# Performance work log

Measured on AMD Instinct MI355X. Metric: run time of the kernel, lower is better.

The kernel has to match this reference:

```python
import jax, jax.numpy as jnp
import numpy as np

B, N, S = 4, 16384, 16384
C1, C2 = 256, 256
D_MODEL, NHEAD, OUT_DIM = 256, 8, 256
HEAD_DIM = D_MODEL // NHEAD
EPS_ATTN = 1e-6


def _layernorm(x, g, b, eps=1e-5):
    mu = jnp.mean(x, axis=-1, keepdims=True)
    var = jnp.mean(jnp.square(x - mu), axis=-1, keepdims=True)
    return (x - mu) * jax.lax.rsqrt(var + eps) * g + b


def setup_inputs() -> dict:
    key = jax.random.key(0)
    ks = jax.random.split(key, 20)
    def w(k, shape, fan_in):
        return jax.random.normal(k, shape, jnp.float32) * (1.0 / np.sqrt(fan_in))
    return {
        "feat1": jax.random.normal(ks[0], (B, C1, N), jnp.float32),
        "xyz1": jax.random.normal(ks[1], (B, N, 3), jnp.float32),
        "feat2": jax.random.normal(ks[2], (B, C2, S), jnp.float32),
        "xyz2": jax.random.normal(ks[3], (B, S, 3), jnp.float32),
        # pos_mlp2: Linear(3, d_model) -> ReLU -> Linear(d_model, feat2_dim)
        "pos_w1": w(ks[4], (D_MODEL, 3), 3),
        "pos_b1": jnp.zeros((D_MODEL,), jnp.float32),
        "pos_w2": w(ks[5], (C2, D_MODEL), D_MODEL),
        "pos_b2": jnp.zeros((C2,), jnp.float32),
        "q_w": w(ks[6], (D_MODEL, C1), C1),
        "k_w": w(ks[7], (D_MODEL, C2), C2),
        "v_w": w(ks[8], (D_MODEL, C2), C2),
        "merge_w": w(ks[9], (D_MODEL, D_MODEL), D_MODEL),
        # mlp: Linear(C1 + d_model, 2*d_model) -> ReLU -> Linear(2*d_model, out_dim)
        "mlp_w1": w(ks[10], (2 * D_MODEL, C1 + D_MODEL), C1 + D_MODEL),
        "mlp_w2": w(ks[11], (OUT_DIM, 2 * D_MODEL), 2 * D_MODEL),
        "ln1_g": jnp.ones((D_MODEL,), jnp.float32),
        "ln1_b": jnp.zeros((D_MODEL,), jnp.float32),
        "ln2_g": jnp.ones((OUT_DIM,), jnp.float32),
        "ln2_b": jnp.zeros((OUT_DIM,), jnp.float32),
    }


def reference(feat1, xyz1, feat2, xyz2, pos_w1, pos_b1, pos_w2, pos_b2,
              q_w, k_w, v_w, merge_w, mlp_w1, mlp_w2,
              ln1_g, ln1_b, ln2_g, ln2_b):
    bs = feat1.shape[0]
    f1 = jnp.transpose(feat1, (0, 2, 1))  # [B, N, C1]
    f2 = jnp.transpose(feat2, (0, 2, 1))  # [B, S, C2]
    # positional MLP on xyz2 added to feat2
    pos = jax.nn.relu(xyz2 @ pos_w1.T + pos_b1) @ pos_w2.T + pos_b2
    f2p = f2 + pos
    q = (f1 @ q_w.T).reshape(bs, -1, NHEAD, HEAD_DIM)   # [B, N, H, D]
    k = (f2 @ k_w.T).reshape(bs, -1, NHEAD, HEAD_DIM)   # [B, S, H, D]
    v = (f2p @ v_w.T).reshape(bs, -1, NHEAD, HEAD_DIM)  # [B, S, H, D]
    # Linear attention (elu feature map)
    Q = jax.nn.elu(q) + 1.0
    K = jax.nn.elu(k) + 1.0
    v_len = v.shape[1]
    V = v / v_len
    KV = jnp.einsum('nshd,nshv->nhdv', K, V)                 # [B, H, D, D]
    Z = 1.0 / (jnp.einsum('nlhd,nhd->nlh', Q, K.sum(axis=1)) + EPS_ATTN)
    msg = jnp.einsum('nlhd,nhdv,nlh->nlhv', Q, KV, Z) * v_len  # [B, N, H, D]
    msg = msg.reshape(bs, -1, NHEAD * HEAD_DIM) @ merge_w.T
    msg = _layernorm(msg, ln1_g, ln1_b)
    msg = jnp.concatenate([f1, msg], axis=2)
    msg = jax.nn.relu(msg @ mlp_w1.T) @ mlp_w2.T
    msg = _layernorm(msg, ln2_g, ln2_b)
    return jnp.transpose(msg, (0, 2, 1))  # [B, out_dim, N]
```

## Files before the change

kernel.cpp:

```cpp
#include <hip/hip_runtime.h>


typedef float f32x4 __attribute__((ext_vector_type(4)));
typedef __bf16 bf16x8 __attribute__((ext_vector_type(8)));
typedef __bf16 bf16x4 __attribute__((ext_vector_type(4)));

#define MFMA16(a, b, c) __builtin_amdgcn_mfma_f32_16x16x32_bf16((a), (b), (c), 0, 0, 0)

__device__ __forceinline__ void gll16(const __bf16* g, __bf16* l) {
    __builtin_amdgcn_global_load_lds(
        (const __attribute__((address_space(1))) void*)g,
        (__attribute__((address_space(3))) void*)l, 16, 0, 0);
}

__global__ __launch_bounds__(256) void prep_weights_kernel(
    const float* __restrict__ s0, const float* __restrict__ s1,
    const float* __restrict__ s2, const float* __restrict__ s3,
    const float* __restrict__ s4, const float* __restrict__ s5,
    const float* __restrict__ s6,
    __bf16* __restrict__ d0, __bf16* __restrict__ d1, __bf16* __restrict__ d2,
    __bf16* __restrict__ d3, __bf16* __restrict__ d4, __bf16* __restrict__ d5,
    __bf16* __restrict__ d6, float* __restrict__ zbase)
{
    int idx = blockIdx.x * 256 + threadIdx.x;
    if (idx < 327680) {
        int seg = idx >> 16, off = idx & 65535;
        const float* s = (seg == 0) ? s0 : (seg == 1) ? s1 : (seg == 2) ? s2 : (seg == 3) ? s3 : s4;
        __bf16* d = (seg == 0) ? d0 : (seg == 1) ? d1 : (seg == 2) ? d2 : (seg == 3) ? d3 : d4;
        d[off] = (__bf16)s[off];
    } else if (idx < 589824) {
        int off = idx - 327680; d5[off] = (__bf16)s5[off];
    } else if (idx < 720896) {
        int off = idx - 589824; d6[off] = (__bf16)s6[off];
    } else if (idx < 754688) {
        zbase[idx - 720896] = 0.f;
    }
}

__global__ __launch_bounds__(256) void pos_hidden_kernel(
    const float* __restrict__ xyz2, const float* __restrict__ pw1,
    const float* __restrict__ pb1, __bf16* __restrict__ Hid)
{
    const int tid = threadIdx.x;
    size_t tok = (size_t)blockIdx.x * 8 + (tid >> 5);
    int c0 = (tid & 31) * 8;
    const float* xz = xyz2 + tok * 3;
    float x = xz[0], y = xz[1], z = xz[2];
    bf16x8 o;
    #pragma unroll
    for (int j = 0; j < 8; ++j) {
        const float* wr = pw1 + (size_t)(c0 + j) * 3;
        float h = fmaf(x, wr[0], fmaf(y, wr[1], fmaf(z, wr[2], pb1[c0 + j])));
        o[j] = (__bf16)fmaxf(h, 0.f);
    }
    *(bf16x8*)(Hid + tok * 256 + c0) = o;
}

__global__ __launch_bounds__(256) void transpose_cast_kernel(
    const float* __restrict__ In, __bf16* __restrict__ Outb)
{
    const int tid = threadIdx.x;
    const int t0 = blockIdx.x * 64, c0 = blockIdx.y * 64;
    const size_t b = blockIdx.z;
    __shared__ __bf16 tile[64 * 72];
    #pragma unroll
    for (int i = 0; i < 4; ++i) {
        int c = i * 16 + (tid >> 4);
        int t4 = (tid & 15) * 4;
        float4 v = *(const float4*)(In + (b * 256 + c0 + c) * 16384 + t0 + t4);
        tile[(t4 + 0) * 72 + c] = (__bf16)v.x;
        tile[(t4 + 1) * 72 + c] = (__bf16)v.y;
        tile[(t4 + 2) * 72 + c] = (__bf16)v.z;
        tile[(t4 + 3) * 72 + c] = (__bf16)v.w;
    }
    __syncthreads();
    #pragma unroll
    for (int i = 0; i < 2; ++i) {
        int chunk = tid + i * 256;
        int tr = chunk >> 3, c8 = (chunk & 7) * 8;
        bf16x8 v = *(const bf16x8*)(tile + tr * 72 + c8);
        *(bf16x8*)(Outb + (b * 16384 + t0 + tr) * 256 + c0 + c8) = v;
    }
}

enum { EPI_STORE = 0, EPI_ELU = 1, EPI_ADDB = 2, EPI_RELU = 3, EPI_ELU_KSUM = 4 };

template <int EPI, bool SPLIT>
__global__ __launch_bounds__(256, 4) void gemm_tok(
    const __bf16* __restrict__ Wg,
    const __bf16* __restrict__ A0,
    const __bf16* __restrict__ A1,
    __bf16* __restrict__ Outg,
    const float* __restrict__ bias,
    const __bf16* __restrict__ addg,
    float* __restrict__ KSg,
    int K, int Cout)
{
    const int tid = threadIdx.x, w = tid >> 6, l = tid & 63, lm = l & 15;
    const int gm0 = blockIdx.x * 128, gn0 = blockIdx.y * 128;
    const size_t b = blockIdx.z;
    const __bf16* A0b = A0 + b * 16384 * (size_t)256;
    const __bf16* A1b = SPLIT ? (A1 + b * 16384 * (size_t)256) : nullptr;
    __bf16* Outb = Outg + b * 16384 * (size_t)Cout;
    const __bf16* addb = (EPI == EPI_ADDB) ? (addg + b * 16384 * (size_t)256) : nullptr;

    __shared__ __bf16 Alds[2][128 * 32];
    __shared__ __bf16 Wlds[2][128 * 32];
    __shared__ float kred[16 * 64];

    f32x4 acc[4][4];
    #pragma unroll
    for (int i = 0; i < 4; ++i)
        #pragma unroll
        for (int j = 0; j < 4; ++j) acc[i][j] = (f32x4){0.f, 0.f, 0.f, 0.f};

    const int wm = (w >> 1) * 64, wn = (w & 1) * 64;
    const int srow = tid >> 2, scol = (tid & 3) * 8;
    const int koff = (l >> 4) * 8;
    const int wbase = w * 512;

    auto stage = [&](int buf, int ks) {
        const __bf16* As = A0b; int kk = ks;
        if (SPLIT && ks >= 256) { As = A1b; kk = ks - 256; }
        gll16(As + (size_t)(gm0 + srow) * 256 + kk + scol,      &Alds[buf][wbase]);
        gll16(As + (size_t)(gm0 + 64 + srow) * 256 + kk + scol, &Alds[buf][2048 + wbase]);
        gll16(Wg + (size_t)(gn0 + srow) * K + ks + scol,        &Wlds[buf][wbase]);
        gll16(Wg + (size_t)(gn0 + 64 + srow) * K + ks + scol,   &Wlds[buf][2048 + wbase]);
    };

    stage(0, 0);
    __syncthreads();
    int cur = 0;
    for (int ks = 0; ks < K; ks += 32) {
        if (ks + 32 < K) stage(cur ^ 1, ks + 32);
        bf16x8 af[4], wf[4];
        #pragma unroll
        for (int mf = 0; mf < 4; ++mf)
            af[mf] = *(const bf16x8*)&Alds[cur][(wm + mf * 16 + lm) * 32 + koff];
        #pragma unroll
        for (int nf = 0; nf < 4; ++nf)
            wf[nf] = *(const bf16x8*)&Wlds[cur][(wn + nf * 16 + lm) * 32 + koff];
        #pragma unroll
        for (int mf = 0; mf < 4; ++mf)
            #pragma unroll
            for (int nf = 0; nf < 4; ++nf)
                acc[mf][nf] = MFMA16(af[mf], wf[nf], acc[mf][nf]);
        __syncthreads();
        cur ^= 1;
    }

    const int r0 = (l >> 4) * 4;
    float kpart[4] = {0.f, 0.f, 0.f, 0.f};
    #pragma unroll
    for (int mf = 0; mf < 4; ++mf) {
        #pragma unroll
        for (int nf = 0; nf < 4; ++nf) {
            int tok = gm0 + wm + mf * 16 + r0;
            int ch  = gn0 + wn + nf * 16 + lm;
            #pragma unroll
            for (int r = 0; r < 4; ++r) {
                float v = acc[mf][nf][r];
                if (EPI == EPI_ELU || EPI == EPI_ELU_KSUM)
                    v = (v > 0.f) ? (v + 1.f) : __expf(v);
                if (EPI == EPI_RELU) v = fmaxf(v, 0.f);
                if (EPI == EPI_ADDB) v = v + bias[ch] + (float)addb[(size_t)(tok + r) * 256 + ch];
                if (EPI == EPI_ELU_KSUM) kpart[nf] += v;
                Outb[(size_t)(tok + r) * Cout + ch] = (__bf16)v;
            }
        }
    }
    if (EPI == EPI_ELU_KSUM) {
        #pragma unroll
        for (int nf = 0; nf < 4; ++nf)
            kred[(w * 4 + (l >> 4)) * 64 + nf * 16 + lm] = kpart[nf];
        __syncthreads();
        if (tid < 128) {
            int c = tid;
            int wsel = (c >= 64) ? 1 : 0;
            float s = 0.f;
            #pragma unroll
            for (int q = 0; q < 4; ++q)
                s += kred[((wsel * 4) + q) * 64 + (c & 63)]
                   + kred[(((wsel + 2) * 4) + q) * 64 + (c & 63)];
            atomicAdd(&KSg[b * 256 + gn0 + c], s);
        }
    }
}

__global__ __launch_bounds__(256) void kv_kernel(
    const __bf16* __restrict__ Kb, const __bf16* __restrict__ Vb,
    float* __restrict__ KVg)
{
    const int tid = threadIdx.x, w = tid >> 6, l = tid & 63, lm = l & 15;
    const int sc = blockIdx.x, h = blockIdx.y, b = blockIdx.z;
    __shared__ __bf16 kT[32 * 264];
    __shared__ __bf16 vT[32 * 264];
    __shared__ float red[4 * 32 * 32];

    f32x4 acc[2][2];
    #pragma unroll
    for (int i = 0; i < 2; ++i)
        #pragma unroll
        for (int j = 0; j < 2; ++j) acc[i][j] = (f32x4){0.f, 0.f, 0.f, 0.f};

    const int koff = (l >> 4) * 8, r0 = (l >> 4) * 4;
    const size_t rowbase = (size_t)b * 16384;
    bf16x4 kreg[8], vreg[8];
    auto loadsub = [&](int sub) {
        int s0 = sc * 1024 + sub * 256;
        #pragma unroll
        for (int pass = 0; pass < 8; ++pass) {
            int sl = pass * 32 + (tid >> 3);
            int c4 = (tid & 7) * 4;
            kreg[pass] = *(const bf16x4*)(Kb + (rowbase + s0 + sl) * 256 + h * 32 + c4);
            vreg[pass] = *(const bf16x4*)(Vb + (rowbase + s0 + sl) * 256 + h * 32 + c4);
        }
    };
    loadsub(0);
    for (int sub = 0; sub < 4; ++sub) {
        __syncthreads();
        #pragma unroll
        for (int pass = 0; pass < 8; ++pass) {
            int sl = pass * 32 + (tid >> 3);
            int c4 = (tid & 7) * 4;
            #pragma unroll
            for (int i = 0; i < 4; ++i) {
                kT[(c4 + i) * 264 + sl] = kreg[pass][i];
                vT[(c4 + i) * 264 + sl] = vreg[pass][i];
            }
        }
        __syncthreads();
        if (sub < 3) loadsub(sub + 1);
        #pragma unroll
        for (int kq = 0; kq < 2; ++kq) {
            int sb = w * 64 + kq * 32;
            bf16x8 af[2], bfr[2];
            #pragma unroll
            for (int mf = 0; mf < 2; ++mf)
                af[mf] = *(const bf16x8*)(kT + (mf * 16 + lm) * 264 + sb + koff);
            #pragma unroll
            for (int nf = 0; nf < 2; ++nf)
                bfr[nf] = *(const bf16x8*)(vT + (nf * 16 + lm) * 264 + sb + koff);
            #pragma unroll
            for (int mf = 0; mf < 2; ++mf)
                #pragma unroll
                for (int nf = 0; nf < 2; ++nf)
                    acc[mf][nf] = MFMA16(af[mf], bfr[nf], acc[mf][nf]);
        }
    }
    #pragma unroll
    for (int mf = 0; mf < 2; ++mf)
        #pragma unroll
        for (int nf = 0; nf < 2; ++nf)
            #pragma unroll
            for (int r = 0; r < 4; ++r) {
                int d = mf * 16 + r0 + r, e = nf * 16 + lm;
                red[w * 1024 + d * 32 + e] = acc[mf][nf][r];
            }
    __syncthreads();
    #pragma unroll
    for (int i = 0; i < 4; ++i) {
        int idx = tid + i * 256;
        float s = red[idx] + red[1024 + idx] + red[2048 + idx] + red[3072 + idx];
        atomicAdd(&KVg[((size_t)(b * 8 + h)) * 1024 + idx], s);
    }
}

__global__ __launch_bounds__(256) void attn_apply(
    const __bf16* __restrict__ Qb, const float* __restrict__ KVg,
    const float* __restrict__ KSg, __bf16* __restrict__ Msg)
{
    const int tid = threadIdx.x, w = tid >> 6, l = tid & 63, lm = l & 15;
    const int tok0 = blockIdx.x * 64;
    const size_t b = blockIdx.y;
    __shared__ __bf16 kvT[8 * 32 * 40];
    __shared__ float ks_lds[256], z_lds[64 * 8];

    const float* KVb = KVg + b * 8192;
    #pragma unroll
    for (int i = 0; i < 32; ++i) {
        int idx = tid + i * 256;
        int h = idx >> 10, d = (idx >> 5) & 31, e = idx & 31;
        kvT[(h * 32 + e) * 40 + d] = (__bf16)KVb[idx];
    }
    ks_lds[tid] = KSg[b * 256 + tid];
    __syncthreads();

    const __bf16* Qbase = Qb + (b * 16384 + tok0) * (size_t)256;
    #pragma unroll
    for (int i = 0; i < 2; ++i) {
        int p = tid + i * 256;
        int tok = p >> 3, h = p & 7;
        const __bf16* qr = Qbase + (size_t)tok * 256 + h * 32;
        float s = 0.f;
        #pragma unroll
        for (int j = 0; j < 4; ++j) {
            bf16x8 q8 = *(const bf16x8*)(qr + j * 8);
            #pragma unroll
            for (int t = 0; t < 8; ++t) s += (float)q8[t] * ks_lds[h * 32 + j * 8 + t];
        }
        z_lds[tok * 8 + h] = 1.f / (s + 1e-6f);
    }
    __syncthreads();

    const int koff = (l >> 4) * 8, r0 = (l >> 4) * 4;
    const f32x4 zero4 = (f32x4){0.f, 0.f, 0.f, 0.f};
    #pragma unroll
    for (int h = 0; h < 8; ++h) {
        bf16x8 af = *(const bf16x8*)(Qbase + (size_t)(w * 16 + lm) * 256 + h * 32 + koff);
        #pragma unroll
        for (int nf = 0; nf < 2; ++nf) {
            bf16x8 bv = *(const bf16x8*)(kvT + (h * 32 + nf * 16 + lm) * 40 + koff);
            f32x4 m = MFMA16(af, bv, zero4);
            #pragma unroll
            for (int r = 0; r < 4; ++r) {
                int tok = w * 16 + r0 + r;
                Msg[(b * 16384 + tok0 + tok) * (size_t)256 + h * 32 + nf * 16 + lm] =
                    (__bf16)(m[r] * z_lds[tok * 8 + h]);
            }
        }
    }
}

template <bool TRANS>
__global__ __launch_bounds__(256, 2) void gemm_ln(
    const __bf16* __restrict__ Ag,
    const __bf16* __restrict__ Wg,
    const float* __restrict__ gv, const float* __restrict__ bv,
    __bf16* __restrict__ OutB,
    float* __restrict__ OutF,
    int K)
{
    const int tid = threadIdx.x, w = tid >> 6, l = tid & 63, lm = l & 15;
    const int tok0 = blockIdx.x * 128;
    const size_t b = blockIdx.y;
    const size_t trow = b * 16384 + tok0;

    __shared__ __align__(16) char smem[49152];
    __bf16* AldsB = (__bf16*)smem;
    __bf16* WldsB = (__bf16*)(smem + 16384);
    __shared__ float red1[512], red2[512], mu_lds[128], rs_lds[128];
    __shared__ float g_lds[256], b_lds[256];
    g_lds[tid] = gv[tid];
    b_lds[tid] = bv[tid];

    f32x4 acc[8][4];
    #pragma unroll
    for (int i = 0; i < 8; ++i)
        #pragma unroll
        for (int j = 0; j < 4; ++j) acc[i][j] = (f32x4){0.f, 0.f, 0.f, 0.f};

    const int srow = tid >> 2, scol = (tid & 3) * 8;
    const int koff = (l >> 4) * 8, wn = w * 64, wbase = w * 512;

    auto stage = [&](int buf, int ks) {
        gll16(Ag + (trow + srow) * K + ks + scol,      AldsB + buf * 4096 + wbase);
        gll16(Ag + (trow + 64 + srow) * K + ks + scol, AldsB + buf * 4096 + 2048 + wbase);
        #pragma unroll
        for (int c = 0; c < 4; ++c)
            gll16(Wg + (size_t)(c * 64 + srow) * K + ks + scol,
                  WldsB + buf * 8192 + c * 2048 + wbase);
    };

    stage(0, 0);
    __syncthreads();
    int cur = 0;
    for (int ks = 0; ks < K; ks += 32) {
        if (ks + 32 < K) stage(cur ^ 1, ks + 32);
        bf16x8 af[8], wf[4];
        #pragma unroll
        for (int mf = 0; mf < 8; ++mf)
            af[mf] = *(const bf16x8*)(AldsB + cur * 4096 + (mf * 16 + lm) * 32 + koff);
        #pragma unroll
        for (int nf = 0; nf < 4; ++nf)
            wf[nf] = *(const bf16x8*)(WldsB + cur * 8192 + (wn + nf * 16 + lm) * 32 + koff);
        #pragma unroll
        for (int mf = 0; mf < 8; ++mf)
            #pragma unroll
            for (int nf = 0; nf < 4; ++nf)
                acc[mf][nf] = MFMA16(af[mf], wf[nf], acc[mf][nf]);
        __syncthreads();
        cur ^= 1;
    }

    const int r0 = (l >> 4) * 4;
    #pragma unroll
    for (int mf = 0; mf < 8; ++mf) {
        #pragma unroll
        for (int r = 0; r < 4; ++r) {
            float s1 = 0.f, s2 = 0.f;
            #pragma unroll
            for (int nf = 0; nf < 4; ++nf) { float v = acc[mf][nf][r]; s1 += v; s2 += v * v; }
            #pragma unroll
            for (int m = 1; m < 16; m <<= 1) { s1 += __shfl_xor(s1, m, 64); s2 += __shfl_xor(s2, m, 64); }
            if (lm == 0) {
                red1[w * 128 + mf * 16 + r0 + r] = s1;
                red2[w * 128 + mf * 16 + r0 + r] = s2;
            }
        }
    }
    __syncthreads();
    if (tid < 128) {
        float s1 = red1[tid] + red1[128 + tid] + red1[256 + tid] + red1[384 + tid];
        float s2 = red2[tid] + red2[128 + tid] + red2[256 + tid] + red2[384 + tid];
        float mu = s1 * (1.f / 256.f);
        mu_lds[tid] = mu;
        rs_lds[tid] = rsqrtf(s2 * (1.f / 256.f) - mu * mu + 1e-5f);
    }
    __syncthreads();

    if (TRANS) {
        float* wb = (float*)smem + w * 2112;
        #pragma unroll
        for (int nf = 0; nf < 4; ++nf) {
            __syncthreads();
            float gg = g_lds[wn + nf * 16 + lm], bb = b_lds[wn + nf * 16 + lm];
            #pragma unroll
            for (int mf = 0; mf < 8; ++mf) {
                int tl = mf * 16 + r0;
                f32x4 v;
                #pragma unroll
                for (int r = 0; r < 4; ++r)
                    v[r] = (acc[mf][nf][r] - mu_lds[tl + r]) * rs_lds[tl + r] * gg + bb;
                *(f32x4*)(wb + lm * 132 + tl) = v;
            }
            __syncthreads();
            #pragma unroll
            for (int t = 0; t < 8; ++t) {
                int row = t * 2 + (l >> 5);
                int col = (l & 31) * 4;
                f32x4 v = *(const f32x4*)(wb + row * 132 + col);
                *(f32x4*)(OutF + (b * 256 + wn + nf * 16 + row) * (size_t)16384 + tok0 + col) = v;
            }
        }
    } else {
        #pragma unroll
        for (int mf = 0; mf < 8; ++mf) {
            #pragma unroll
            for (int nf = 0; nf < 4; ++nf) {
                int ch = wn + nf * 16 + lm;
                #pragma unroll
                for (int r = 0; r < 4; ++r) {
                    int tl = mf * 16 + r0 + r;
                    float y = (acc[mf][nf][r] - mu_lds[tl]) * rs_lds[tl] * g_lds[ch] + b_lds[ch];
                    OutB[(trow + tl) * (size_t)256 + ch] = (__bf16)y;
                }
            }
        }
    }
}

extern "C" void kernel_launch(void* const* d_in, const int* in_sizes, int n_in,
                              void* d_out, int out_size, void* d_ws, size_t ws_size,
                              hipStream_t stream) {
    const float* feat1   = (const float*)d_in[0];
    const float* feat2   = (const float*)d_in[2];
    const float* xyz2    = (const float*)d_in[3];
    const float* pos_w1  = (const float*)d_in[4];
    const float* pos_b1  = (const float*)d_in[5];
    const float* pos_w2  = (const float*)d_in[6];
    const float* pos_b2  = (const float*)d_in[7];
    const float* q_w     = (const float*)d_in[8];
    const float* k_w     = (const float*)d_in[9];
    const float* v_w     = (const float*)d_in[10];
    const float* merge_w = (const float*)d_in[11];
    const float* mlp_w1  = (const float*)d_in[12];
    const float* mlp_w2  = (const float*)d_in[13];
    const float* ln1_g   = (const float*)d_in[14];
    const float* ln1_b   = (const float*)d_in[15];
    const float* ln2_g   = (const float*)d_in[16];
    const float* ln2_b   = (const float*)d_in[17];
    float* outp = (float*)d_out;

    char* ws = (char*)d_ws;
    size_t off = 0;
    auto alloc = [&](size_t bytes) { char* p = ws + off; off += (bytes + 255) & ~(size_t)255; return p; };
    const size_t ACT = (size_t)4 * 16384 * 256 * 2;
    __bf16* WQ  = (__bf16*)alloc(65536 * 2);
    __bf16* WK  = (__bf16*)alloc(65536 * 2);
    __bf16* WV  = (__bf16*)alloc(65536 * 2);
    __bf16* WM  = (__bf16*)alloc(65536 * 2);
    __bf16* WP2 = (__bf16*)alloc(65536 * 2);
    __bf16* W1  = (__bf16*)alloc(262144 * 2);
    __bf16* W2  = (__bf16*)alloc(131072 * 2);
    float*  KV  = (float*)alloc(4 * 8 * 32 * 32 * 4);
    float*  KS  = (float*)alloc(4 * 256 * 4);
    __bf16* F1T = (__bf16*)alloc(ACT);
    __bf16* HID = (__bf16*)alloc(ACT);
    __bf16* F2T = (__bf16*)alloc(ACT);
    __bf16* F2P = (__bf16*)alloc(ACT);
    __bf16* KB  = (__bf16*)alloc(ACT);
    __bf16* VB  = (__bf16*)alloc(ACT);
    __bf16* QB  = (__bf16*)alloc(ACT);
    __bf16* H1     = HID;
    __bf16* MSGRAW = F2T;
    __bf16* MSG1   = F2P;
    if (ws_size < off) return;

    prep_weights_kernel<<<2948, 256, 0, stream>>>(q_w, k_w, v_w, merge_w, pos_w2,
                                                  mlp_w1, mlp_w2,
                                                  WQ, WK, WV, WM, WP2, W1, W2, KV);
    pos_hidden_kernel<<<8192, 256, 0, stream>>>(xyz2, pos_w1, pos_b1, HID);
    transpose_cast_kernel<<<dim3(256, 4, 4), 256, 0, stream>>>(feat1, F1T);
    transpose_cast_kernel<<<dim3(256, 4, 4), 256, 0, stream>>>(feat2, F2T);
    gemm_tok<EPI_ADDB, false><<<dim3(128, 2, 4), 256, 0, stream>>>(WP2, HID, nullptr, F2P, pos_b2, F2T, nullptr, 256, 256);
    gemm_tok<EPI_ELU_KSUM, false><<<dim3(128, 2, 4), 256, 0, stream>>>(WK, F2T, nullptr, KB, nullptr, nullptr, KS, 256, 256);
    gemm_tok<EPI_STORE, false><<<dim3(128, 2, 4), 256, 0, stream>>>(WV, F2P, nullptr, VB, nullptr, nullptr, nullptr, 256, 256);
    gemm_tok<EPI_ELU, false><<<dim3(128, 2, 4), 256, 0, stream>>>(WQ, F1T, nullptr, QB, nullptr, nullptr, nullptr, 256, 256);
    kv_kernel<<<dim3(16, 8, 4), 256, 0, stream>>>(KB, VB, KV);
    attn_apply<<<dim3(256, 4), 256, 0, stream>>>(QB, KV, KS, MSGRAW);
    gemm_ln<false><<<dim3(128, 4), 256, 0, stream>>>(MSGRAW, WM, ln1_g, ln1_b, MSG1, nullptr, 256);
    gemm_tok<EPI_RELU, true><<<dim3(128, 4, 4), 256, 0, stream>>>(W1, F1T, MSG1, H1, nullptr, nullptr, nullptr, 512, 512);
    gemm_ln<true><<<dim3(128, 4), 256, 0, stream>>>(H1, W2, ln2_g, ln2_b, nullptr, outp, 512);
    (void)in_sizes; (void)n_in; (void)out_size;
}
```

Baseline: 454.2 us.

## Add weight-resident K=256 GEMM kernel with 4-slot swizzled A pipeline

Introduces a new 512-thread kernel for the four K=256 projection GEMMs. Each block loads its full 128-channel weight slice into LDS once, with an XOR swizzle, and streams 512 tokens through a 4-slot A ring buffer that uses explicit vmcnt waits and a single barrier per step. This cuts repeated weight traffic and the double-buffer sync overhead of the old gemm_tok. The price is one block per CU with large LDS use and lower occupancy. The buffer aliasing is also reshuffled, and gemm_tok is reduced to the ReLU-only split case.

After: 575.4 us. +26.7%, slower.

```diff
diff --git a/kernel.cpp b/kernel.cpp
--- a/kernel.cpp
+++ b/kernel.cpp
@@ -83,17 +83,270 @@
     }
 }
 
-enum { EPI_STORE = 0, EPI_ELU = 1, EPI_ADDB = 2, EPI_RELU = 3, EPI_ELU_KSUM = 4 };
-
-template <int EPI, bool SPLIT>
+enum { EPI_STORE = 0, EPI_ELU = 1, EPI_ADDB = 2, EPI_ELU_KSUM = 4 };
+
+template <int EPI>
+__global__ __launch_bounds__(512, 1) void rib(
+    const __bf16* __restrict__ Wg,
+    const __bf16* __restrict__ Ag,
+    __bf16* __restrict__ Og,
+    const float* __restrict__ bias,
+    const __bf16* __restrict__ resg,
+    float* __restrict__ KSg)
+{
+    const int tid = threadIdx.x, w = tid >> 6, l = tid & 63, lm = l & 15;
+    const int n0 = blockIdx.y * 128;
+    const size_t b = blockIdx.z;
+    const size_t tokbase = b * 16384 + (size_t)blockIdx.x * 512;
+    const __bf16* Ab = Ag + tokbase * 256;
+    __bf16* Ob = Og + tokbase * 256;
+    const __bf16* Rb = (EPI == EPI_ADDB) ? (resg + tokbase * 256) : nullptr;
+
+    __shared__ __bf16 Asl[4][8192];
+    __shared__ __bf16 Wl[32768];
+    __shared__ float kred[16][128];
+
+    #pragma unroll
+    for (int j = 0; j < 8; ++j) {
+        int inst = w * 8 + j;
+        int chl = inst * 2 + (l >> 5);
+        int c8 = (l & 31) ^ (chl & 7);
+        gll16(Wg + (size_t)(n0 + chl) * 256 + c8 * 8, Wl + inst * 512);
+    }
+
+    auto stageA = [&](int slot, int gk) {
+        int t = gk >> 3; if (t > 1) t = 1;
+        int kk = (gk & 7) * 32;
+        const __bf16* src = Ab + (size_t)t * 65536;
+        #pragma unroll
+        for (int j = 0; j < 2; ++j) {
+            int rbase = (w * 2 + j) * 16;
+            int row = rbase + (l >> 2);
+            int c8 = (l & 3) ^ ((row >> 1) & 3);
+            gll16(src + (size_t)row * 256 + kk + c8 * 8, Asl[slot] + rbase * 32);
+        }
+    };
+
+    stageA(0, 0);
+    stageA(1, 1);
+    asm volatile("s_waitcnt vmcnt(2)" ::: "memory");
+    __builtin_amdgcn_s_barrier();
+    asm volatile("" ::: "memory");
+
+    const int wm = (w >> 1) * 64, wn = (w & 1) * 64;
+    const int r0 = (l >> 4) * 4;
+    float kpart[4] = {0.f, 0.f, 0.f, 0.f};
+
+    for (int t = 0; t < 2; ++t) {
+        f32x4 acc[4][4];
+        #pragma unroll
+        for (int i = 0; i < 4; ++i)
+            #pragma unroll
+            for (int j = 0; j < 4; ++j) acc[i][j] = (f32x4){0.f, 0.f, 0.f, 0.f};
+
+        for (int i = 0; i < 8; ++i) {
+            int g = t * 8 + i;
+            stageA((g + 2) & 3, g + 2);
+            asm volatile("s_waitcnt vmcnt(4)" ::: "memory");
+            __builtin_amdgcn_s_barrier();
+            asm volatile("" ::: "memory");
+            const __bf16* As = &Asl[g & 3][0];
+            bf16x8 af[4], wf[4];
+            #pragma unroll
+            for (int mf = 0; mf < 4; ++mf) {
+                int row = wm + mf * 16 + lm;
+                int c8 = ((l >> 4) ^ (row >> 1)) & 3;
+                af[mf] = *(const bf16x8*)(As + row * 32 + c8 * 8);
+            }
+            #pragma unroll
+            for (int nf = 0; nf < 4; ++nf) {
+                int chl = wn + nf * 16 + lm;
+                int c8 = (i * 4 + (l >> 4)) ^ (chl & 7);
+                wf[nf] = *(const bf16x8*)(Wl + chl * 256 + c8 * 8);
+            }
+            #pragma unroll
+            for (int mf = 0; mf < 4; ++mf)
+                #pragma unroll
+                for (int nf = 0; nf < 4; ++nf)
+                    acc[mf][nf] = MFMA16(af[mf], wf[nf], acc[mf][nf]);
+        }
+
+        __bf16* Ot = Ob + (size_t)t * 65536;
+        const __bf16* Rt = (EPI == EPI_ADDB) ? (Rb + (size_t)t * 65536) : nullptr;
+        #pragma unroll
+        for (int mf = 0; mf < 4; ++mf) {
+            #pragma unroll
+            for (int nf = 0; nf < 4; ++nf) {
+                int ch = n0 + wn + nf * 16 + lm;
+                #pragma unroll
+                for (int r = 0; r < 4; ++r) {
+                    int tokl = wm + mf * 16 + r0 + r;
+                    float v = acc[mf][nf][r];
+                    if (EPI == EPI_ELU || EPI == EPI_ELU_KSUM)
+                        v = (v > 0.f) ? (v + 1.f) : __expf(v);
+                    if (EPI == EPI_ADDB)
+                        v = v + bias[ch] + (float)Rt[(size_t)tokl * 256 + ch];
+                    if (EPI == EPI_ELU_KSUM) kpart[nf] += v;
+                    Ot[(size_t)tokl * 256 + ch] = (__bf16)v;
+                }
+            }
+        }
+    }
+
+    if (EPI == EPI_ELU_KSUM) {
+        __syncthreads();
+        #pragma unroll
+        for (int nf = 0; nf < 4; ++nf)
+            kred[(w >> 1) * 4 + (l >> 4)][wn + nf * 16 + lm] = kpart[nf];
+        __syncthreads();
+        if (tid < 128) {
+            float s = 0.f;
+            #pragma unroll
+            for (int rr = 0; rr < 16; ++rr) s += kred[rr][tid];
+            atomicAdd(&KSg[b * 256 + n0 + tid], s);
+        }
+    }
+}
+
+__global__ __launch_bounds__(256) void kv_kernel(
+    const __bf16* __restrict__ Kb, const __bf16* __restrict__ Vb,
+    float* __restrict__ KVg)
+{
+    const int tid = threadIdx.x, w = tid >> 6, l = tid & 63, lm = l & 15;
+    const int sc = blockIdx.x, h = blockIdx.y, b = blockIdx.z;
+    __shared__ __bf16 kT[32 * 264];
+    __shared__ __bf16 vT[32 * 264];
+    __shared__ float red[4 * 32 * 32];
+
+    f32x4 acc[2][2];
+    #pragma unroll
+    for (int i = 0; i < 2; ++i)
+        #pragma unroll
+        for (int j = 0; j < 2; ++j) acc[i][j] = (f32x4){0.f, 0.f, 0.f, 0.f};
+
+    const int koff = (l >> 4) * 8, r0 = (l >> 4) * 4;
+    const size_t rowbase = (size_t)b * 16384;
+    bf16x4 kreg[8], vreg[8];
+    auto loadsub = [&](int sub) {
+        int s0 = sc * 1024 + sub * 256;
+        #pragma unroll
+        for (int pass = 0; pass < 8; ++pass) {
+            int sl = pass * 32 + (tid >> 3);
+            int c4 = (tid & 7) * 4;
+            kreg[pass] = *(const bf16x4*)(Kb + (rowbase + s0 + sl) * 256 + h * 32 + c4);
+            vreg[pass] = *(const bf16x4*)(Vb + (rowbase + s0 + sl) * 256 + h * 32 + c4);
+        }
+    };
+    loadsub(0);
+    for (int sub = 0; sub < 4; ++sub) {
+        __syncthreads();
+        #pragma unroll
+        for (int pass = 0; pass < 8; ++pass) {
+            int sl = pass * 32 + (tid >> 3);
+            int c4 = (tid & 7) * 4;
+            #pragma unroll
+            for (int i = 0; i < 4; ++i) {
+                kT[(c4 + i) * 264 + sl] = kreg[pass][i];
+                vT[(c4 + i) * 264 + sl] = vreg[pass][i];
+            }
+        }
+        __syncthreads();
+        if (sub < 3) loadsub(sub + 1);
+        #pragma unroll
+        for (int kq = 0; kq < 2; ++kq) {
+            int sb = w * 64 + kq * 32;
+            bf16x8 af[2], bfr[2];
+            #pragma unroll
+            for (int mf = 0; mf < 2; ++mf)
+                af[mf] = *(const bf16x8*)(kT + (mf * 16 + lm) * 264 + sb + koff);
+            #pragma unroll
+            for (int nf = 0; nf < 2; ++nf)
+                bfr[nf] = *(const bf16x8*)(vT + (nf * 16 + lm) * 264 + sb + koff);
+            #pragma unroll
+            for (int mf = 0; mf < 2; ++mf)
+                #pragma unroll
+                for (int nf = 0; nf < 2; ++nf)
+                    acc[mf][nf] = MFMA16(af[mf], bfr[nf], acc[mf][nf]);
+        }
+    }
+    #pragma unroll
+    for (int mf = 0; mf < 2; ++mf)
+        #pragma unroll
+        for (int nf = 0; nf < 2; ++nf)
+            #pragma unroll
+            for (int r = 0; r < 4; ++r) {
+                int d = mf * 16 + r0 + r, e = nf * 16 + lm;
+                red[w * 1024 + d * 32 + e] = acc[mf][nf][r];
+            }
+    __syncthreads();
+    #pragma unroll
+    for (int i = 0; i < 4; ++i) {
+        int idx = tid + i * 256;
+        float s = red[idx] + red[1024 + idx] + red[2048 + idx] + red[3072 + idx];
+        atomicAdd(&KVg[((size_t)(b * 8 + h)) * 1024 + idx], s);
+    }
+}
+
+__global__ __launch_bounds__(256) void attn_apply(
+    const __bf16* __restrict__ Qb, const float* __restrict__ KVg,
+    const float* __restrict__ KSg, __bf16* __restrict__ Msg)
+{
+    const int tid = threadIdx.x, w = tid >> 6, l = tid & 63, lm = l & 15;
+    const int tok0 = blockIdx.x * 64;
+    const size_t b = blockIdx.y;
+    __shared__ __bf16 kvT[8 * 32 * 40];
+    __shared__ float ks_lds[256], z_lds[64 * 8];
+
+    const float* KVb = KVg + b * 8192;
+    #pragma unroll
+    for (int i = 0; i < 32; ++i) {
+        int idx = tid + i * 256;
+        int h = idx >> 10, d = (idx >> 5) & 31, e = idx & 31;
+        kvT[(h * 32 + e) * 40 + d] = (__bf16)KVb[idx];
+    }
+    ks_lds[tid] = KSg[b * 256 + tid];
+    __syncthreads();
+
+    const __bf16* Qbase = Qb + (b * 16384 + tok0) * (size_t)256;
+    #pragma unroll
+    for (int i = 0; i < 2; ++i) {
+        int p = tid + i * 256;
+        int tok = p >> 3, h = p & 7;
+        const __bf16* qr = Qbase + (size_t)tok * 256 + h * 32;
+        float s = 0.f;
+        #pragma unroll
+        for (int j = 0; j < 4; ++j) {
+            bf16x8 q8 = *(const bf16x8*)(qr + j * 8);
+            #pragma unroll
+            for (int t = 0; t < 8; ++t) s += (float)q8[t] * ks_lds[h * 32 + j * 8 + t];
+        }
+        z_lds[tok * 8 + h] = 1.f / (s + 1e-6f);
+    }
+    __syncthreads();
+
+    const int koff = (l >> 4) * 8, r0 = (l >> 4) * 4;
+    const f32x4 zero4 = (f32x4){0.f, 0.f, 0.f, 0.f};
+    #pragma unroll
+    for (int h = 0; h < 8; ++h) {
+        bf16x8 af = *(const bf16x8*)(Qbase + (size_t)(w * 16 + lm) * 256 + h * 32 + koff);
+        #pragma unroll
+        for (int nf = 0; nf < 2; ++nf) {
+            bf16x8 bv = *(const bf16x8*)(kvT + (h * 32 + nf * 16 + lm) * 40 + koff);
+            f32x4 m = MFMA16(af, bv, zero4);
+            #pragma unroll
+            for (int r = 0; r < 4; ++r) {
+                int tok = w * 16 + r0 + r;
+                Msg[(b * 16384 + tok0 + tok) * (size_t)256 + h * 32 + nf * 16 + lm] =
+                    (__bf16)(m[r] * z_lds[tok * 8 + h]);
+            }
+        }
+    }
+}
+
+template <int EPI_UNUSED, bool SPLIT>
 __global__ __launch_bounds__(256, 4) void gemm_tok(
-    const __bf16* __restrict__ Wg,
-    const __bf16* __restrict__ A0,
-    const __bf16* __restrict__ A1,
-    __bf16* __restrict__ Outg,
-    const float* __restrict__ bias,
-    const __bf16* __restrict__ addg,
-    float* __restrict__ KSg,
+    const __bf16* __restrict__ Wg, const __bf16* __restrict__ A0,
+    const __bf16* __restrict__ A1, __bf16* __restrict__ Outg,
     int K, int Cout)
 {
     const int tid = threadIdx.x, w = tid >> 6, l = tid & 63, lm = l & 15;
@@ -102,11 +355,9 @@
     const __bf16* A0b = A0 + b * 16384 * (size_t)256;
     const __bf16* A1b = SPLIT ? (A1 + b * 16384 * (size_t)256) : nullptr;
     __bf16* Outb = Outg + b * 16384 * (size_t)Cout;
-    const __bf16* addb = (EPI == EPI_ADDB) ? (addg + b * 16384 * (size_t)256) : nullptr;
 
     __shared__ __bf16 Alds[2][128 * 32];
     __shared__ __bf16 Wlds[2][128 * 32];
-    __shared__ float kred[16 * 64];
 
     f32x4 acc[4][4];
     #pragma unroll
@@ -150,186 +401,23 @@
     }
 
     const int r0 = (l >> 4) * 4;
-    float kpart[4] = {0.f, 0.f, 0.f, 0.f};
-    #pragma unroll
-    for (int mf = 0; mf < 4; ++mf) {
+    #pragma unroll
+    for (int mf = 0; mf < 4; ++mf)
         #pragma unroll
         for (int nf = 0; nf < 4; ++nf) {
             int tok = gm0 + wm + mf * 16 + r0;
             int ch  = gn0 + wn + nf * 16 + lm;
             #pragma unroll
-            for (int r = 0; r < 4; ++r) {
-                float v = acc[mf][nf][r];
-                if (EPI == EPI_ELU || EPI == EPI_ELU_KSUM)
-                    v = (v > 0.f) ? (v + 1.f) : __expf(v);
-                if (EPI == EPI_RELU) v = fmaxf(v, 0.f);
-                if (EPI == EPI_ADDB) v = v + bias[ch] + (float)addb[(size_t)(tok + r) * 256 + ch];
-                if (EPI == EPI_ELU_KSUM) kpart[nf] += v;
-                Outb[(size_t)(tok + r) * Cout + ch] = (__bf16)v;
-            }
-        }
-    }
-    if (EPI == EPI_ELU_KSUM) {
-        #pragma unroll
-        for (int nf = 0; nf < 4; ++nf)
-            kred[(w * 4 + (l >> 4)) * 64 + nf * 16 + lm] = kpart[nf];
-        __syncthreads();
-        if (tid < 128) {
-            int c = tid;
-            int wsel = (c >= 64) ? 1 : 0;
-            float s = 0.f;
-            #pragma unroll
-            for (int q = 0; q < 4; ++q)
-                s += kred[((wsel * 4) + q) * 64 + (c & 63)]
-                   + kred[(((wsel + 2) * 4) + q) * 64 + (c & 63)];
-            atomicAdd(&KSg[b * 256 + gn0 + c], s);
-        }
-    }
-}
-
-__global__ __launch_bounds__(256) void kv_kernel(
-    const __bf16* __restrict__ Kb, const __bf16* __restrict__ Vb,
-    float* __restrict__ KVg)
-{
-    const int tid = threadIdx.x, w = tid >> 6, l = tid & 63, lm = l & 15;
-    const int sc = blockIdx.x, h = blockIdx.y, b = blockIdx.z;
-    __shared__ __bf16 kT[32 * 264];
-    __shared__ __bf16 vT[32 * 264];
-    __shared__ float red[4 * 32 * 32];
-
-    f32x4 acc[2][2];
-    #pragma unroll
-    for (int i = 0; i < 2; ++i)
-        #pragma unroll
-        for (int j = 0; j < 2; ++j) acc[i][j] = (f32x4){0.f, 0.f, 0.f, 0.f};
-
-    const int koff = (l >> 4) * 8, r0 = (l >> 4) * 4;
-    const size_t rowbase = (size_t)b * 16384;
-    bf16x4 kreg[8], vreg[8];
-    auto loadsub = [&](int sub) {
-        int s0 = sc * 1024 + sub * 256;
-        #pragma unroll
-        for (int pass = 0; pass < 8; ++pass) {
-            int sl = pass * 32 + (tid >> 3);
-            int c4 = (tid & 7) * 4;
-            kreg[pass] = *(const bf16x4*)(Kb + (rowbase + s0 + sl) * 256 + h * 32 + c4);
-            vreg[pass] = *(const bf16x4*)(Vb + (rowbase + s0 + sl) * 256 + h * 32 + c4);
-        }
-    };
-    loadsub(0);
-    for (int sub = 0; sub < 4; ++sub) {
-        __syncthreads();
-        #pragma unroll
-        for (int pass = 0; pass < 8; ++pass) {
-            int sl = pass * 32 + (tid >> 3);
-            int c4 = (tid & 7) * 4;
-            #pragma unroll
-            for (int i = 0; i < 4; ++i) {
-                kT[(c4 + i) * 264 + sl] = kreg[pass][i];
-                vT[(c4 + i) * 264 + sl] = vreg[pass][i];
-            }
-        }
-        __syncthreads();
-        if (sub < 3) loadsub(sub + 1);
-        #pragma unroll
-        for (int kq = 0; kq < 2; ++kq) {
-            int sb = w * 64 + kq * 32;
-            bf16x8 af[2], bfr[2];
-            #pragma unroll
-            for (int mf = 0; mf < 2; ++mf)
-                af[mf] = *(const bf16x8*)(kT + (mf * 16 + lm) * 264 + sb + koff);
-            #pragma unroll
-            for (int nf = 0; nf < 2; ++nf)
-                bfr[nf] = *(const bf16x8*)(vT + (nf * 16 + lm) * 264 + sb + koff);
-            #pragma unroll
-            for (int mf = 0; mf < 2; ++mf)
-                #pragma unroll
-                for (int nf = 0; nf < 2; ++nf)
-                    acc[mf][nf] = MFMA16(af[mf], bfr[nf], acc[mf][nf]);
-        }
-    }
-    #pragma unroll
-    for (int mf = 0; mf < 2; ++mf)
-        #pragma unroll
-        for (int nf = 0; nf < 2; ++nf)
-            #pragma unroll
-            for (int r = 0; r < 4; ++r) {
-                int d = mf * 16 + r0 + r, e = nf * 16 + lm;
-                red[w * 1024 + d * 32 + e] = acc[mf][nf][r];
-            }
-    __syncthreads();
-    #pragma unroll
-    for (int i = 0; i < 4; ++i) {
-        int idx = tid + i * 256;
-        float s = red[idx] + red[1024 + idx] + red[2048 + idx] + red[3072 + idx];
-        atomicAdd(&KVg[((size_t)(b * 8 + h)) * 1024 + idx], s);
-    }
-}
-
-__global__ __launch_bounds__(256) void attn_apply(
-    const __bf16* __restrict__ Qb, const float* __restrict__ KVg,
-    const float* __restrict__ KSg, __bf16* __restrict__ Msg)
-{
-    const int tid = threadIdx.x, w = tid >> 6, l = tid & 63, lm = l & 15;
-    const int tok0 = blockIdx.x * 64;
-    const size_t b = blockIdx.y;
-    __shared__ __bf16 kvT[8 * 32 * 40];
-    __shared__ float ks_lds[256], z_lds[64 * 8];
-
-    const float* KVb = KVg + b * 8192;
-    #pragma unroll
-    for (int i = 0; i < 32; ++i) {
-        int idx = tid + i * 256;
-        int h = idx >> 10, d = (idx >> 5) & 31, e = idx & 31;
-        kvT[(h * 32 + e) * 40 + d] = (__bf16)KVb[idx];
-    }
-    ks_lds[tid] = KSg[b * 256 + tid];
-    __syncthreads();
-
-    const __bf16* Qbase = Qb + (b * 16384 + tok0) * (size_t)256;
-    #pragma unroll
-    for (int i = 0; i < 2; ++i) {
-        int p = tid + i * 256;
-        int tok = p >> 3, h = p & 7;
-        const __bf16* qr = Qbase + (size_t)tok * 256 + h * 32;
-        float s = 0.f;
-        #pragma unroll
-        for (int j = 0; j < 4; ++j) {
-            bf16x8 q8 = *(const bf16x8*)(qr + j * 8);
-            #pragma unroll
-            for (int t = 0; t < 8; ++t) s += (float)q8[t] * ks_lds[h * 32 + j * 8 + t];
-        }
-        z_lds[tok * 8 + h] = 1.f / (s + 1e-6f);
-    }
-    __syncthreads();
-
-    const int koff = (l >> 4) * 8, r0 = (l >> 4) * 4;
-    const f32x4 zero4 = (f32x4){0.f, 0.f, 0.f, 0.f};
-    #pragma unroll
-    for (int h = 0; h < 8; ++h) {
-        bf16x8 af = *(const bf16x8*)(Qbase + (size_t)(w * 16 + lm) * 256 + h * 32 + koff);
-        #pragma unroll
-        for (int nf = 0; nf < 2; ++nf) {
-            bf16x8 bv = *(const bf16x8*)(kvT + (h * 32 + nf * 16 + lm) * 40 + koff);
-            f32x4 m = MFMA16(af, bv, zero4);
-            #pragma unroll
-            for (int r = 0; r < 4; ++r) {
-                int tok = w * 16 + r0 + r;
-                Msg[(b * 16384 + tok0 + tok) * (size_t)256 + h * 32 + nf * 16 + lm] =
-                    (__bf16)(m[r] * z_lds[tok * 8 + h]);
-            }
-        }
-    }
+            for (int r = 0; r < 4; ++r)
+                Outb[(size_t)(tok + r) * Cout + ch] = (__bf16)fmaxf(acc[mf][nf][r], 0.f);
+        }
 }
 
 template <bool TRANS>
 __global__ __launch_bounds__(256, 2) void gemm_ln(
-    const __bf16* __restrict__ Ag,
-    const __bf16* __restrict__ Wg,
+    const __bf16* __restrict__ Ag, const __bf16* __restrict__ Wg,
     const float* __restrict__ gv, const float* __restrict__ bv,
-    __bf16* __restrict__ OutB,
-    float* __restrict__ OutF,
-    int K)
+    __bf16* __restrict__ OutB, float* __restrict__ OutF, int K)
 {
     const int tid = threadIdx.x, w = tid >> 6, l = tid & 63, lm = l & 15;
     const int tok0 = blockIdx.x * 128;
@@ -486,15 +574,15 @@
     float*  KV  = (float*)alloc(4 * 8 * 32 * 32 * 4);
     float*  KS  = (float*)alloc(4 * 256 * 4);
     __bf16* F1T = (__bf16*)alloc(ACT);
+    __bf16* F2T = (__bf16*)alloc(ACT);
     __bf16* HID = (__bf16*)alloc(ACT);
-    __bf16* F2T = (__bf16*)alloc(ACT);
     __bf16* F2P = (__bf16*)alloc(ACT);
     __bf16* KB  = (__bf16*)alloc(ACT);
     __bf16* VB  = (__bf16*)alloc(ACT);
-    __bf16* QB  = (__bf16*)alloc(ACT);
-    __bf16* H1     = HID;
-    __bf16* MSGRAW = F2T;
-    __bf16* MSG1   = F2P;
+    __bf16* QB     = HID;
+    __bf16* MSGRAW = F2P;
+    __bf16* MSG1   = F2T;
+    __bf16* H1     = KB;
     if (ws_size < off) return;
 
     prep_weights_kernel<<<2948, 256, 0, stream>>>(q_w, k_w, v_w, merge_w, pos_w2,
@@ -503,14 +591,14 @@
     pos_hidden_kernel<<<8192, 256, 0, stream>>>(xyz2, pos_w1, pos_b1, HID);
     transpose_cast_kernel<<<dim3(256, 4, 4), 256, 0, stream>>>(feat1, F1T);
     transpose_cast_kernel<<<dim3(256, 4, 4), 256, 0, stream>>>(feat2, F2T);
-    gemm_tok<EPI_ADDB, false><<<dim3(128, 2, 4), 256, 0, stream>>>(WP2, HID, nullptr, F2P, pos_b2, F2T, nullptr, 256, 256);
-    gemm_tok<EPI_ELU_KSUM, false><<<dim3(128, 2, 4), 256, 0, stream>>>(WK, F2T, nullptr, KB, nullptr, nullptr, KS, 256, 256);
-    gemm_tok<EPI_STORE, false><<<dim3(128, 2, 4), 256, 0, stream>>>(WV, F2P, nullptr, VB, nullptr, nullptr, nullptr, 256, 256);
-    gemm_tok<EPI_ELU, false><<<dim3(128, 2, 4), 256, 0, stream>>>(WQ, F1T, nullptr, QB, nullptr, nullptr, nullptr, 256, 256);
+    rib<EPI_ADDB><<<dim3(32, 2, 4), 512, 0, stream>>>(WP2, HID, F2P, pos_b2, F2T, nullptr);
+    rib<EPI_ELU_KSUM><<<dim3(32, 2, 4), 512, 0, stream>>>(WK, F2T, KB, nullptr, nullptr, KS);
+    rib<EPI_STORE><<<dim3(32, 2, 4), 512, 0, stream>>>(WV, F2P, VB, nullptr, nullptr, nullptr);
+    rib<EPI_ELU><<<dim3(32, 2, 4), 512, 0, stream>>>(WQ, F1T, QB, nullptr, nullptr, nullptr);
     kv_kernel<<<dim3(16, 8, 4), 256, 0, stream>>>(KB, VB, KV);
     attn_apply<<<dim3(256, 4), 256, 0, stream>>>(QB, KV, KS, MSGRAW);
     gemm_ln<false><<<dim3(128, 4), 256, 0, stream>>>(MSGRAW, WM, ln1_g, ln1_b, MSG1, nullptr, 256);
-    gemm_tok<EPI_RELU, true><<<dim3(128, 4, 4), 256, 0, stream>>>(W1, F1T, MSG1, H1, nullptr, nullptr, nullptr, 512, 512);
+    gemm_tok<0, true><<<dim3(128, 4, 4), 256, 0, stream>>>(W1, F1T, MSG1, H1, 512, 512);
     gemm_ln<true><<<dim3(128, 4), 256, 0, stream>>>(H1, W2, ln2_g, ln2_b, nullptr, outp, 512);
     (void)in_sizes; (void)n_in; (void)out_size;
 }
```
